# Performance work log

Measured on AMD Instinct MI355X. Metric: run time of the kernel, lower is better.

Reference implementation:

```python
import jax, jax.numpy as jnp
import numpy as np


def _lstm(x, Wih, Whh, bih, bhh):
    # x: [B, T, D_in]; PyTorch gate order: i, f, g, o. Returns all hidden states [B, T, H].
    B = x.shape[0]
    H = Whh.shape[1]
    b = bih + bhh  # [4H]
    xs = jnp.transpose(x, (1, 0, 2))  # [T, B, D_in] for scan over time

    def step(carry, xt):
        h, c = carry
        gates = xt @ Wih.T + h @ Whh.T + b  # [B, 4H]
        i, f, g, o = jnp.split(gates, 4, axis=-1)
        i = jax.nn.sigmoid(i)
        f = jax.nn.sigmoid(f)
        g = jnp.tanh(g)
        o = jax.nn.sigmoid(o)
        c = f * c + i * g
        h = o * jnp.tanh(c)
        return (h, c), h

    h0 = jnp.zeros((B, H), dtype=x.dtype)
    c0 = jnp.zeros((B, H), dtype=x.dtype)
    _, hs = jax.lax.scan(step, (h0, c0), xs)  # hs: [T, B, H]
    return jnp.transpose(hs, (1, 0, 2))  # [B, T, H]


def setup_inputs() -> dict:
    key = jax.random.key(0)
    ks = jax.random.split(key, 11)
    B, T, D_IN, H1, H2, NC = 256, 2048, 16, 5, 50, 20

    def u(k, shape, fan):
        bound = 1.0 / np.sqrt(fan)
        return jax.random.uniform(k, shape, jnp.float32, -bound, bound)

    x = jax.random.normal(ks[0], (B, T, D_IN), dtype=jnp.float32)
    return {
        "x": x,
        "W1ih": u(ks[1], (4 * H1, D_IN), H1),
        "W1hh": u(ks[2], (4 * H1, H1), H1),
        "b1ih": u(ks[3], (4 * H1,), H1),
        "b1hh": u(ks[4], (4 * H1,), H1),
        "W2ih": u(ks[5], (4 * H2, H1), H2),
        "W2hh": u(ks[6], (4 * H2, H2), H2),
        "b2ih": u(ks[7], (4 * H2,), H2),
        "b2hh": u(ks[8], (4 * H2,), H2),
        "Wfc": u(ks[9], (NC, H2), H2),
        "bfc": u(ks[10], (NC,), H2),
    }


def reference(x, W1ih, W1hh, b1ih, b1hh, W2ih, W2hh, b2ih, b2hh, Wfc, bfc):
    h1 = _lstm(x, W1ih, W1hh, b1ih, b1hh)      # [B, T, 5]
    h2 = _lstm(h1, W2ih, W2hh, b2ih, b2hh)     # [B, T, 50]
    # Dropout(p=0.2) in eval mode == identity (deterministic reference)
    last = h2[:, -1, :]                        # [B, 50]
    result = last @ Wfc.T + bfc                # [B, num_classes]
    return (result, last)
```

## Files before the change

### kernel.cpp

```cpp
#include <hip/hip_runtime.h>
#include <math.h>

namespace {

constexpr int TSEQ   = 2048;
constexpr int DIN    = 16;
constexpr int NH1    = 5;
constexpr int NH2    = 50;
constexpr int NCLS   = 20;
constexpr int CHUNK  = 64;
constexpr int NCHUNK = TSEQ / CHUNK;
constexpr int BATCH  = 256;
constexpr int GSTR   = 80;
constexpr int PROW   = 4 * GSTR;

__device__ __forceinline__ float fast_sigm(float x) {
    return __fdividef(1.f, 1.f + __expf(-x));
}
__device__ __forceinline__ float fast_tanh(float x) {
    return fmaf(2.f, fast_sigm(2.f * x), -1.f);
}

template <int CTRL>
__device__ __forceinline__ float qperm(float v) {
    int i = __builtin_bit_cast(int, v);
    int r = __builtin_amdgcn_update_dpp(i, i, CTRL, 0xf, 0xf, false);
    return __builtin_bit_cast(float, r);
}
__device__ __forceinline__ float rdlane(float v, int lane) {
    return __builtin_bit_cast(float,
        __builtin_amdgcn_readlane(__builtin_bit_cast(int, v), lane));
}

#define W4_BARRIER() asm volatile("s_waitcnt lgkmcnt(0)\n\ts_barrier" ::: "memory")

template <int N> struct IC { static constexpr int v = N; };

__global__ __launch_bounds__(320, 1) void lstm_fused_kernel(
    const float* __restrict__ x,
    const float* __restrict__ W1ih,
    const float* __restrict__ W1hh,
    const float* __restrict__ b1ih,
    const float* __restrict__ b1hh,
    const float* __restrict__ W2ih,
    const float* __restrict__ W2hh,
    const float* __restrict__ b2ih,
    const float* __restrict__ b2hh,
    const float* __restrict__ Wfc,
    const float* __restrict__ bfc,
    float* __restrict__ out)
{
    const int b    = blockIdx.x;
    const int tid  = threadIdx.x;
    const int lane = tid & 63;
    const int wv   = tid >> 6;

    __shared__ __align__(16) float s_x[2][CHUNK * DIN];
    __shared__ __align__(16) float s_part[2][4][PROW];
    __shared__ __align__(16) float s_h1[2][CHUNK][8];
    __shared__ float s_h2[NH2];

    const float* xb = x + (size_t)b * TSEQ * DIN;

    if (wv == 4) {
        const int r1 = (lane < NCLS) ? ((lane & 3) * NH1 + (lane >> 2)) : 0;
        float w1h[NH1], w1x[DIN];
        #pragma unroll
        for (int j = 0; j < NH1; ++j) w1h[j] = W1hh[r1 * NH1 + j];
        #pragma unroll
        for (int d = 0; d < DIN; ++d) w1x[d] = W1ih[r1 * DIN + d];
        const float bias1 = b1ih[r1] + b1hh[r1];
        const bool  isg1  = ((lane & 3) == 2) && (lane < NCLS);
        const float isc1  = isg1 ? 2.f : 1.f;
        const float osc1  = isg1 ? 2.f : 1.f;
        const float off1  = isg1 ? -1.f : 0.f;
        float c1 = 0.f;
        float sh0v = 0.f, sh1v = 0.f, sh2v = 0.f, sh3v = 0.f, sh4v = 0.f;
        float4 xr0, xr1, xr2, xr3;

        auto l1_prod = [&](const float* xs, float* h1out) {
            float4 xv0 = *(const float4*)(xs + 0);
            float4 xv1 = *(const float4*)(xs + 4);
            float4 xv2 = *(const float4*)(xs + 8);
            float4 xv3 = *(const float4*)(xs + 12);
            float sa = fmaf(xv0.y, w1x[1],  xv0.x * w1x[0]);
            sa = fmaf(xv0.z, w1x[2], sa);  sa = fmaf(xv0.w, w1x[3], sa);
            float sb = fmaf(xv1.y, w1x[5],  xv1.x * w1x[4]);
            sb = fmaf(xv1.z, w1x[6], sb);  sb = fmaf(xv1.w, w1x[7], sb);
            float sc = fmaf(xv2.y, w1x[9],  xv2.x * w1x[8]);
            sc = fmaf(xv2.z, w1x[10], sc); sc = fmaf(xv2.w, w1x[11], sc);
            float sd = fmaf(xv3.y, w1x[13], xv3.x * w1x[12]);
            sd = fmaf(xv3.z, w1x[14], sd); sd = fmaf(xv3.w, w1x[15], sd);
            float ha = fmaf(sh1v, w1h[1], sh0v * w1h[0]);
            ha = fmaf(sh2v, w1h[2], ha);
            float hb = fmaf(sh4v, w1h[4], sh3v * w1h[3]);
            float g1 = ((sa + sb) + (sc + sd)) + ((ha + hb) + bias1);
            float act = fmaf(osc1, fast_sigm(isc1 * g1), off1);
            float f_ = qperm<0xB1>(act);
            float gg = qperm<0x4E>(act);
            float o_ = qperm<0x1B>(act);
            c1 = fmaf(f_, c1, act * gg);
            float h1me = o_ * fast_tanh(c1);
            sh0v = rdlane(h1me, 0);  sh1v = rdlane(h1me, 4);
            sh2v = rdlane(h1me, 8);  sh3v = rdlane(h1me, 12);
            sh4v = rdlane(h1me, 16);
            if ((lane & 3) == 0 && lane < NCLS) h1out[lane >> 2] = h1me;
        };

        xr0 = ((const float4*)(xb))[lane];
        xr1 = ((const float4*)(xb + 256))[lane];
        xr2 = ((const float4*)(xb + 512))[lane];
        xr3 = ((const float4*)(xb + 768))[lane];
        ((float4*)s_x[0])[lane]       = xr0;
        ((float4*)s_x[0])[64 + lane]  = xr1;
        ((float4*)s_x[0])[128 + lane] = xr2;
        ((float4*)s_x[0])[192 + lane] = xr3;
        for (int t = 0; t < CHUNK; ++t)
            l1_prod(&s_x[0][t * DIN], &s_h1[0][t][0]);
        xr0 = ((const float4*)(xb + 1024))[lane];
        xr1 = ((const float4*)(xb + 1280))[lane];
        xr2 = ((const float4*)(xb + 1536))[lane];
        xr3 = ((const float4*)(xb + 1792))[lane];
        ((float4*)s_x[1])[lane]       = xr0;
        ((float4*)s_x[1])[64 + lane]  = xr1;
        ((float4*)s_x[1])[128 + lane] = xr2;
        ((float4*)s_x[1])[192 + lane] = xr3;
        xr0 = ((const float4*)(xb + 2048))[lane];
        xr1 = ((const float4*)(xb + 2304))[lane];
        xr2 = ((const float4*)(xb + 2560))[lane];
        xr3 = ((const float4*)(xb + 2816))[lane];
        W4_BARRIER();

        #pragma unroll 1
        for (int c = 0; c < NCHUNK; ++c) {
            const int  cur   = c & 1, nxt = cur ^ 1;
            const bool w4run = (c + 1 < NCHUNK);
            if (c + 2 < NCHUNK) {
                ((float4*)s_x[cur])[lane]       = xr0;
                ((float4*)s_x[cur])[64 + lane]  = xr1;
                ((float4*)s_x[cur])[128 + lane] = xr2;
                ((float4*)s_x[cur])[192 + lane] = xr3;
                if (c + 3 < NCHUNK) {
                    const float* xc = xb + (size_t)(c + 3) * (CHUNK * DIN);
                    xr0 = ((const float4*)(xc))[lane];
                    xr1 = ((const float4*)(xc + 256))[lane];
                    xr2 = ((const float4*)(xc + 512))[lane];
                    xr3 = ((const float4*)(xc + 768))[lane];
                }
            }
            #pragma unroll 1
            for (int tt = 0; tt < CHUNK; tt += 2) {
                if (w4run) l1_prod(&s_x[nxt][tt * DIN], &s_h1[nxt][tt][0]);
                W4_BARRIER();
                if (w4run) l1_prod(&s_x[nxt][(tt + 1) * DIN], &s_h1[nxt][tt + 1][0]);
                W4_BARRIER();
            }
        }
    } else {
        auto l2loop = [&](auto cntc, auto offc) {
            constexpr int CNT = decltype(cntc)::v;
            constexpr int OFF = decltype(offc)::v;

            float wpw[4][CNT];
            #pragma unroll
            for (int i = 0; i < 4; ++i) {
                const int pr = 4 * lane + i;
                const int pg = pr >> 6;
                const int pu = pr & 63;
                #pragma unroll
                for (int kk = 0; kk < CNT; ++kk)
                    wpw[i][kk] = (pu < NH2) ? W2hh[(pg * NH2 + pu) * NH2 + (OFF + kk)]
                                            : 0.f;
            }

            const int  ul  = lane >> 2;
            const int  g   = lane & 3;
            const bool onc = (ul < CNT);
            const int  u   = OFF + (onc ? ul : 0);
            float w2i[NH1];
            float bias2 = 0.f;
            if (onc) {
                const int rr = g * NH2 + u;
                #pragma unroll
                for (int d = 0; d < NH1; ++d) w2i[d] = W2ih[rr * NH1 + d];
                bias2 = b2ih[rr] + b2hh[rr];
            } else {
                #pragma unroll
                for (int d = 0; d < NH1; ++d) w2i[d] = 0.f;
            }
            const bool  isg2 = (g == 2);
            const float isc2 = isg2 ? 2.f : 1.f;
            const float osc2 = isg2 ? 2.f : 1.f;
            const float off2 = isg2 ? -1.f : 0.f;

            float4* wpart = (float4*)(&s_part[0][wv][GSTR * (lane >> 4)]) + (lane & 15);
            const float* rpart = &s_part[0][0][g * GSTR + u];

            float hsl[CNT];
            #pragma unroll
            for (int k = 0; k < CNT; ++k) hsl[k] = 0.f;
            float c2 = 0.f;
            float4 h1a = make_float4(0.f, 0.f, 0.f, 0.f);
            float  h1e = 0.f;
            float  xp  = 0.f;

            __syncthreads();

            #pragma unroll 1
            for (int c = 0; c < NCHUNK; ++c) {
                const int cur = c & 1;

                #define L2P(BUF, TT)                                           \
                {                                                              \
                    const float* h1p = &s_h1[cur][TT][0];                      \
                    h1a = *(const float4*)h1p;       \
                    h1e = h1p[4];                                              \
                    xp = fmaf(h1a.x, w2i[0], bias2);                           \
                    xp = fmaf(h1a.y, w2i[1], xp);                              \
                    xp = fmaf(h1a.z, w2i[2], xp);                              \
                    xp = fmaf(h1a.w, w2i[3], xp);                              \
                    xp = fmaf(h1e,  w2i[4], xp);                               \
                    float a0 = 0.f, a1 = 0.f, a2 = 0.f, a3 = 0.f;              \
                    _Pragma("unroll")                                          \
                    for (int kk = 0; kk < CNT; ++kk) {                         \
                        a0 = fmaf(hsl[kk], wpw[0][kk], a0);                    \
                        a1 = fmaf(hsl[kk], wpw[1][kk], a1);                    \
                        a2 = fmaf(hsl[kk], wpw[2][kk], a2);                    \
                        a3 = fmaf(hsl[kk], wpw[3][kk], a3);                    \
                    }                                                          \
                    wpart[(BUF) * PROW] = make_float4(a0, a1, a2, a3);         \
                }

                #define L2C(BUF)                                               \
                {                                                              \
                    const float p0 = rpart[(BUF) * (4 * PROW) + 0 * PROW];     \
                    const float p1 = rpart[(BUF) * (4 * PROW) + 1 * PROW];     \
                    const float p2 = rpart[(BUF) * (4 * PROW) + 2 * PROW];     \
                    const float p3 = rpart[(BUF) * (4 * PROW) + 3 * PROW];     \
                    float pre = ((p0 + p1) + (p2 + p3)) + xp;                  \
                    float act2 = fmaf(osc2, fast_sigm(isc2 * pre), off2);      \
                    float v1 = qperm<0xB1>(act2);                              \
                    float v2 = qperm<0x4E>(act2);                              \
                    float v3 = qperm<0x1B>(act2);                              \
                    c2 = fmaf(v1, c2, act2 * v2);                              \
                    float hn = v3 * fast_tanh(c2);                             \
                    _Pragma("unroll")                                          \
                    for (int k = 0; k < CNT; ++k) hsl[k] = rdlane(hn, 4 * k);  \
                }

                #pragma unroll 1
                for (int tt = 0; tt < CHUNK; tt += 2) {
                    L2P(0, tt)
                    __syncthreads();
                    L2C(0)
                    L2P(1, tt + 1)
                    __syncthreads();
                    L2C(1)
                }
                #undef L2P
                #undef L2C
            }

            float hv = 0.f;
            #pragma unroll
            for (int j = 0; j < CNT; ++j)
                if (ul == j) hv = hsl[j];
            if (g == 0 && onc) s_h2[u] = hv;
        };

        if      (wv == 0) l2loop(IC<6>{},  IC<0>{});
        else if (wv == 1) l2loop(IC<15>{}, IC<6>{});
        else if (wv == 2) l2loop(IC<15>{}, IC<21>{});
        else              l2loop(IC<14>{}, IC<36>{});
    }

    __syncthreads();
    if (tid < NH2) out[BATCH * NCLS + b * NH2 + tid] = s_h2[tid];
    if (tid < NCLS) {
        float acc = bfc[tid];
        const float* wr = Wfc + tid * NH2;
        #pragma unroll
        for (int j = 0; j < NH2; ++j) acc = fmaf(s_h2[j], wr[j], acc);
        out[b * NCLS + tid] = acc;
    }
}

}

extern "C" void kernel_launch(void* const* d_in, const int* in_sizes, int n_in,
                              void* d_out, int out_size, void* d_ws, size_t ws_size,
                              hipStream_t stream) {
    (void)in_sizes; (void)n_in; (void)d_ws; (void)ws_size; (void)out_size;
    const float* x    = (const float*)d_in[0];
    const float* W1ih = (const float*)d_in[1];
    const float* W1hh = (const float*)d_in[2];
    const float* b1ih = (const float*)d_in[3];
    const float* b1hh = (const float*)d_in[4];
    const float* W2ih = (const float*)d_in[5];
    const float* W2hh = (const float*)d_in[6];
    const float* b2ih = (const float*)d_in[7];
    const float* b2hh = (const float*)d_in[8];
    const float* Wfc  = (const float*)d_in[9];
    const float* bfc  = (const float*)d_in[10];

    lstm_fused_kernel<<<dim3(BATCH), dim3(320), 0, stream>>>(
        x, W1ih, W1hh, b1ih, b1hh, W2ih, W2hh, b2ih, b2hh, Wfc, bfc,
        (float*)d_out);
}
```

Before: 795.2 us.

## Split layer-2 recurrence across eight waves and use packed FMA

Layer 2's hidden-state matvec is spread over eight waves instead of four, so each wave handles about 4-7 hidden units rather than 6-15. This shortens each wave's serial FMA chain on the per-timestep critical path. The inner accumulation is also rewritten with two-wide packed FMAs. The cost is that each timestep now has to sum eight partials instead of four, the block grows to 576 threads so barriers involve more waves, and shared memory for partials doubles.

```diff
diff --git a/kernel.cpp b/kernel.cpp
--- a/kernel.cpp
+++ b/kernel.cpp
@@ -13,6 +13,10 @@
 constexpr int BATCH  = 256;
 constexpr int GSTR   = 80;
 constexpr int PROW   = 4 * GSTR;
+constexpr int NL2    = 8;
+constexpr int BUFF   = NL2 * PROW;
+
+typedef __attribute__((ext_vector_type(2))) float f32x2;
 
 __device__ __forceinline__ float fast_sigm(float x) {
     return __fdividef(1.f, 1.f + __expf(-x));
@@ -31,12 +35,16 @@
     return __builtin_bit_cast(float,
         __builtin_amdgcn_readlane(__builtin_bit_cast(int, v), lane));
 }
+__device__ __forceinline__ f32x2 pkfma(float s, f32x2 w, f32x2 acc) {
+    f32x2 ss; ss.x = s; ss.y = s;
+    return __builtin_elementwise_fma(ss, w, acc);
+}
 
 #define W4_BARRIER() asm volatile("s_waitcnt lgkmcnt(0)\n\ts_barrier" ::: "memory")
 
 template <int N> struct IC { static constexpr int v = N; };
 
-__global__ __launch_bounds__(320, 1) void lstm_fused_kernel(
+__global__ __launch_bounds__(576, 1) void lstm_fused_kernel(
     const float* __restrict__ x,
     const float* __restrict__ W1ih,
     const float* __restrict__ W1hh,
@@ -56,13 +64,13 @@
     const int wv   = tid >> 6;
 
     __shared__ __align__(16) float s_x[2][CHUNK * DIN];
-    __shared__ __align__(16) float s_part[2][4][PROW];
+    __shared__ __align__(16) float s_part[2][NL2][PROW];
     __shared__ __align__(16) float s_h1[2][CHUNK][8];
     __shared__ float s_h2[NH2];
 
     const float* xb = x + (size_t)b * TSEQ * DIN;
 
-    if (wv == 4) {
+    if (wv == NL2) {
         const int r1 = (lane < NCLS) ? ((lane & 3) * NH1 + (lane >> 2)) : 0;
         float w1h[NH1], w1x[DIN];
         #pragma unroll
@@ -161,16 +169,17 @@
             constexpr int CNT = decltype(cntc)::v;
             constexpr int OFF = decltype(offc)::v;
 
-            float wpw[4][CNT];
+            const int pr0 = 4 * lane;
+            const int pg  = pr0 >> 6;
+            const int pu0 = pr0 & 63;
+            f32x2 wp01[CNT], wp23[CNT];
             #pragma unroll
-            for (int i = 0; i < 4; ++i) {
-                const int pr = 4 * lane + i;
-                const int pg = pr >> 6;
-                const int pu = pr & 63;
-                #pragma unroll
-                for (int kk = 0; kk < CNT; ++kk)
-                    wpw[i][kk] = (pu < NH2) ? W2hh[(pg * NH2 + pu) * NH2 + (OFF + kk)]
-                                            : 0.f;
+            for (int kk = 0; kk < CNT; ++kk) {
+                const int k = OFF + kk;
+                wp01[kk].x = (pu0 + 0 < NH2) ? W2hh[(pg * NH2 + pu0 + 0) * NH2 + k] : 0.f;
+                wp01[kk].y = (pu0 + 1 < NH2) ? W2hh[(pg * NH2 + pu0 + 1) * NH2 + k] : 0.f;
+                wp23[kk].x = (pu0 + 2 < NH2) ? W2hh[(pg * NH2 + pu0 + 2) * NH2 + k] : 0.f;
+                wp23[kk].y = (pu0 + 3 < NH2) ? W2hh[(pg * NH2 + pu0 + 3) * NH2 + k] : 0.f;
             }
 
             const int  ul  = lane >> 2;
@@ -220,24 +229,30 @@
                     xp = fmaf(h1a.z, w2i[2], xp);                              \
                     xp = fmaf(h1a.w, w2i[3], xp);                              \
                     xp = fmaf(h1e,  w2i[4], xp);                               \
-                    float a0 = 0.f, a1 = 0.f, a2 = 0.f, a3 = 0.f;              \
+                    f32x2 a01; a01.x = 0.f; a01.y = 0.f;                       \
+                    f32x2 a23; a23.x = 0.f; a23.y = 0.f;                       \
                     _Pragma("unroll")                                          \
                     for (int kk = 0; kk < CNT; ++kk) {                         \
-                        a0 = fmaf(hsl[kk], wpw[0][kk], a0);                    \
-                        a1 = fmaf(hsl[kk], wpw[1][kk], a1);                    \
-                        a2 = fmaf(hsl[kk], wpw[2][kk], a2);                    \
-                        a3 = fmaf(hsl[kk], wpw[3][kk], a3);                    \
+                        a01 = pkfma(hsl[kk], wp01[kk], a01);                   \
+                        a23 = pkfma(hsl[kk], wp23[kk], a23);                   \
                     }                                                          \
-                    wpart[(BUF) * PROW] = make_float4(a0, a1, a2, a3);         \
+                    wpart[(BUF) * (BUFF / 4)] = make_float4(a01.x, a01.y,      \
+                                                            a23.x, a23.y);     \
                 }
 
                 #define L2C(BUF)                                               \
                 {                                                              \
-                    const float p0 = rpart[(BUF) * (4 * PROW) + 0 * PROW];     \
-                    const float p1 = rpart[(BUF) * (4 * PROW) + 1 * PROW];     \
-                    const float p2 = rpart[(BUF) * (4 * PROW) + 2 * PROW];     \
-                    const float p3 = rpart[(BUF) * (4 * PROW) + 3 * PROW];     \
-                    float pre = ((p0 + p1) + (p2 + p3)) + xp;                  \
+                    const float* rb = rpart + (BUF) * BUFF;                    \
+                    const float p0 = rb[0 * PROW];                             \
+                    const float p1 = rb[1 * PROW];                             \
+                    const float p2 = rb[2 * PROW];                             \
+                    const float p3 = rb[3 * PROW];                             \
+                    const float p4 = rb[4 * PROW];                             \
+                    const float p5 = rb[5 * PROW];                             \
+                    const float p6 = rb[6 * PROW];                             \
+                    const float p7 = rb[7 * PROW];                             \
+                    float pre = (((p0 + p1) + (p2 + p3))                       \
+                               + ((p4 + p5) + (p6 + p7))) + xp;                \
                     float act2 = fmaf(osc2, fast_sigm(isc2 * pre), off2);      \
                     float v1 = qperm<0xB1>(act2);                              \
                     float v2 = qperm<0x4E>(act2);                              \
@@ -268,10 +283,14 @@
             if (g == 0 && onc) s_h2[u] = hv;
         };
 
-        if      (wv == 0) l2loop(IC<6>{},  IC<0>{});
-        else if (wv == 1) l2loop(IC<15>{}, IC<6>{});
-        else if (wv == 2) l2loop(IC<15>{}, IC<21>{});
-        else              l2loop(IC<14>{}, IC<36>{});
+        if      (wv == 0) l2loop(IC<4>{}, IC<0>{});
+        else if (wv == 1) l2loop(IC<7>{}, IC<4>{});
+        else if (wv == 2) l2loop(IC<7>{}, IC<11>{});
+        else if (wv == 3) l2loop(IC<7>{}, IC<18>{});
+        else if (wv == 4) l2loop(IC<4>{}, IC<25>{});
+        else if (wv == 5) l2loop(IC<7>{}, IC<29>{});
+        else if (wv == 6) l2loop(IC<7>{}, IC<36>{});
+        else              l2loop(IC<7>{}, IC<43>{});
     }
 
     __syncthreads();
@@ -303,7 +322,7 @@
     const float* Wfc  = (const float*)d_in[9];
     const float* bfc  = (const float*)d_in[10];
 
-    lstm_fused_kernel<<<dim3(BATCH), dim3(320), 0, stream>>>(
+    lstm_fused_kernel<<<dim3(BATCH), dim3(576), 0, stream>>>(
         x, W1ih, W1hh, b1ih, b1hh, W2ih, W2hh, b2ih, b2hh, Wfc, bfc,
         (float*)d_out);
 }
```

Measured after the change: 1.063 ms. 1.34x slower.
